# Performance work log

Hardware: AMD Instinct MI355X
Metric: run time of the kernel (lower is better)

Reference implementation:

```python
import jax, jax.numpy as jnp
import numpy as np

VOCAB = 50000
EMBED_DIM = 128
REGION = 7
RADIUS = REGION // 2


def setup_inputs() -> dict:
    key = jax.random.key(0)
    k1, k2, k3 = jax.random.split(key, 3)
    vocab_ids = jax.random.randint(k1, (32, 2048), 0, VOCAB, dtype=jnp.int64)
    # word embedding table [V, D]
    word_emb = jax.random.normal(k2, (VOCAB, EMBED_DIM), dtype=jnp.float32) * 0.02
    # context embedding table [V, region_size * D]
    ctx_emb = jax.random.normal(k3, (VOCAB, REGION * EMBED_DIM), dtype=jnp.float32) * 0.02
    return {"vocab_ids": vocab_ids, "word_emb": word_emb, "ctx_emb": ctx_emb}


def reference(vocab_ids, word_emb, ctx_emb):
    # WC (word_context) region embedding.
    B, S = vocab_ids.shape
    L = S - 2 * RADIUS  # actual_length
    trim = vocab_ids[:, RADIUS:S - RADIUS]            # [B, L]
    # sliding-window indices: window i covers positions i..i+REGION-1
    win_pos = jnp.arange(L)[:, None] + jnp.arange(REGION)[None, :]   # [L, R]
    win_ids = vocab_ids[:, win_pos]                    # [B, L, R]
    vocab_e = word_emb[win_ids]                        # [B, L, R, D]
    ctx_e = ctx_emb[trim].reshape(B, L, REGION, EMBED_DIM)  # [B, L, R, D]
    region = jnp.max(vocab_e * ctx_e, axis=2)          # [B, L, D]
    return region
```

## Files before the change

### kernel.cpp

```cpp
#include <hip/hip_runtime.h>
#include <hip/hip_bf16.h>


#define RE_B 32
#define RE_S 2048
#define RE_RAD 3
#define RE_L (RE_S - 2 * RE_RAD)
#define RE_D 128
#define RE_R 7
#define RE_DQ (RE_D / 4)

__global__ __launch_bounds__(256) void region_embed_kernel(
    const int* __restrict__ ids,
    const float4* __restrict__ we,
    const float4* __restrict__ ce,
    float4* __restrict__ out)
{
    const int total = RE_B * RE_L * RE_DQ;
    int idx = blockIdx.x * blockDim.x + threadIdx.x;
    if (idx >= total) return;

    int lane = idx & (RE_DQ - 1);
    int pos  = idx >> 5;
    int b = pos / RE_L;
    int l = pos - b * RE_L;

    const int* row = ids + b * RE_S + l;
    int t = row[RE_RAD];

    const float4* cbase = ce + (size_t)t * (RE_R * RE_DQ) + lane;

    float4 acc;
    acc.x = -INFINITY; acc.y = -INFINITY; acc.z = -INFINITY; acc.w = -INFINITY;

#pragma unroll
    for (int r = 0; r < RE_R; ++r) {
        int w = row[r];
        float4 ve = we[(size_t)w * RE_DQ + lane];
        float4 c  = cbase[r * RE_DQ];
        acc.x = fmaxf(acc.x, ve.x * c.x);
        acc.y = fmaxf(acc.y, ve.y * c.y);
        acc.z = fmaxf(acc.z, ve.z * c.z);
        acc.w = fmaxf(acc.w, ve.w * c.w);
    }

    out[(size_t)pos * RE_DQ + lane] = acc;
}

extern "C" void kernel_launch(void* const* d_in, const int* in_sizes, int n_in,
                              void* d_out, int out_size, void* d_ws, size_t ws_size,
                              hipStream_t stream) {
    const int*    ids = (const int*)d_in[0];
    const float4* we  = (const float4*)d_in[1];
    const float4* ce  = (const float4*)d_in[2];
    float4* out = (float4*)d_out;

    const int total = RE_B * RE_L * RE_DQ;
    const int block = 256;
    const int grid = (total + block - 1) / block;
    region_embed_kernel<<<grid, block, 0, stream>>>(ids, we, ce, out);
}
```

Measured before the change: 50.48 us.

## Process four output positions per thread to reuse word-embedding loads

Each thread now computes KPOS=4 consecutive output positions, loading the 10 overlapping word-embedding rows once and reusing each across up to four windows. This cuts word-embedding gather traffic from 7 loads per output to about 2.5. The ctx_emb gather, which is the bulk of the bytes, is unchanged. Fewer threads are launched and register use per thread rises. The last chunk is clamped to overlap the previous one, so a few positions get written twice with identical values.

```diff
diff --git a/kernel.cpp b/kernel.cpp
--- a/kernel.cpp
+++ b/kernel.cpp
@@ -9,6 +9,8 @@
 #define RE_D 128
 #define RE_R 7
 #define RE_DQ (RE_D / 4)
+#define KPOS 4
+#define NCHUNK ((RE_L + KPOS - 1) / KPOS)
 
 __global__ __launch_bounds__(256) void region_embed_kernel(
     const int* __restrict__ ids,
@@ -16,35 +18,54 @@
     const float4* __restrict__ ce,
     float4* __restrict__ out)
 {
-    const int total = RE_B * RE_L * RE_DQ;
     int idx = blockIdx.x * blockDim.x + threadIdx.x;
-    if (idx >= total) return;
+    int lane  = idx & (RE_DQ - 1);
+    int chunk = idx >> 5;
+    int b = chunk / NCHUNK;
+    int c = chunk - b * NCHUNK;
+    if (b >= RE_B) return;
 
-    int lane = idx & (RE_DQ - 1);
-    int pos  = idx >> 5;
-    int b = pos / RE_L;
-    int l = pos - b * RE_L;
+    int l0 = c * KPOS;
+    if (l0 > RE_L - KPOS) l0 = RE_L - KPOS;
 
-    const int* row = ids + b * RE_S + l;
-    int t = row[RE_RAD];
+    const int* row = ids + b * RE_S + l0;
 
-    const float4* cbase = ce + (size_t)t * (RE_R * RE_DQ) + lane;
+    int wid[KPOS + 6];
+#pragma unroll
+    for (int i = 0; i < KPOS + 6; ++i) wid[i] = row[i];
 
-    float4 acc;
-    acc.x = -INFINITY; acc.y = -INFINITY; acc.z = -INFINITY; acc.w = -INFINITY;
+    const float4* cb[KPOS];
+#pragma unroll
+    for (int k = 0; k < KPOS; ++k)
+        cb[k] = ce + (size_t)wid[k + RE_RAD] * (RE_R * RE_DQ) + lane;
+
+    float4 acc[KPOS];
+#pragma unroll
+    for (int k = 0; k < KPOS; ++k) {
+        acc[k].x = -INFINITY; acc[k].y = -INFINITY;
+        acc[k].z = -INFINITY; acc[k].w = -INFINITY;
+    }
 
 #pragma unroll
-    for (int r = 0; r < RE_R; ++r) {
-        int w = row[r];
-        float4 ve = we[(size_t)w * RE_DQ + lane];
-        float4 c  = cbase[r * RE_DQ];
-        acc.x = fmaxf(acc.x, ve.x * c.x);
-        acc.y = fmaxf(acc.y, ve.y * c.y);
-        acc.z = fmaxf(acc.z, ve.z * c.z);
-        acc.w = fmaxf(acc.w, ve.w * c.w);
+    for (int w = 0; w < KPOS + 6; ++w) {
+        float4 ve = we[(size_t)wid[w] * RE_DQ + lane];
+#pragma unroll
+        for (int k = 0; k < KPOS; ++k) {
+            int r = w - k;
+            if (r >= 0 && r < RE_R) {
+                float4 cv = cb[k][r * RE_DQ];
+                acc[k].x = fmaxf(acc[k].x, ve.x * cv.x);
+                acc[k].y = fmaxf(acc[k].y, ve.y * cv.y);
+                acc[k].z = fmaxf(acc[k].z, ve.z * cv.z);
+                acc[k].w = fmaxf(acc[k].w, ve.w * cv.w);
+            }
+        }
     }
 
-    out[(size_t)pos * RE_DQ + lane] = acc;
+    size_t obase = (size_t)(b * RE_L + l0) * RE_DQ + lane;
+#pragma unroll
+    for (int k = 0; k < KPOS; ++k)
+        out[obase + (size_t)k * RE_DQ] = acc[k];
 }
 
 extern "C" void kernel_launch(void* const* d_in, const int* in_sizes, int n_in,
@@ -55,7 +76,7 @@
     const float4* ce  = (const float4*)d_in[2];
     float4* out = (float4*)d_out;
 
-    const int total = RE_B * RE_L * RE_DQ;
+    const int total = RE_B * NCHUNK * RE_DQ;
     const int block = 256;
     const int grid = (total + block - 1) / block;
     region_embed_kernel<<<grid, block, 0, stream>>>(ids, we, ce, out);
```

New measurement: 50.57 us. No clear change (+0.2%).
